# Kernel optimization log

Measured on AMD Instinct MI355X. Metric: run time of the kernel, lower is better.

## Reference

```python
import jax, jax.numpy as jnp
import numpy as np

NQ = 4          # QUANTUM_QUBITS
DIM = 2 ** NQ   # 16-dim statevector
N_LAYERS = 2
BATCH = 1 << 20


def _bit(idx, w):
    # PennyLane convention: wire 0 is the most-significant bit
    return (idx >> (NQ - 1 - w)) & 1

# Precompute CNOT permutations for the ring (w, (w+1)%NQ): flip target bit when control bit is 1.
_CNOT_PERMS = []
for w in range(NQ):
    c, t = w, (w + 1) % NQ
    perm = np.arange(DIM)
    for idx in range(DIM):
        if _bit(idx, c):
            perm[idx] = idx ^ (1 << (NQ - 1 - t))
    _CNOT_PERMS.append(jnp.asarray(perm))

# Z expectation sign vectors: sign = +1 if bit==0 else -1, per wire -> (NQ, DIM)
_Z_SIGNS = jnp.asarray(
    np.stack([[1.0 - 2.0 * _bit(idx, w) for idx in range(DIM)] for w in range(NQ)]),
    dtype=jnp.float32,
)


def _ry(t):
    c, s = jnp.cos(t / 2), jnp.sin(t / 2)
    return jnp.stack([jnp.stack([c, -s], -1), jnp.stack([s, c], -1)], -2).astype(jnp.complex64)


def _rx(t):
    c = jnp.cos(t / 2).astype(jnp.complex64)
    s = (-1j * jnp.sin(t / 2)).astype(jnp.complex64)
    return jnp.stack([jnp.stack([c, s], -1), jnp.stack([s, c], -1)], -2)


def _rz(t):
    em = jnp.exp(-0.5j * t.astype(jnp.complex64))
    ep = jnp.exp(0.5j * t.astype(jnp.complex64))
    zero = jnp.zeros_like(em)
    return jnp.stack([jnp.stack([em, zero], -1), jnp.stack([zero, ep], -1)], -2)


def _apply_batched(state, g, w):
    # state: (B, DIM); g: (B, 2, 2) per-sample gate on wire w
    s = state.reshape((-1,) + (2,) * NQ)
    s = jnp.moveaxis(s, 1 + w, 1)
    s = jnp.einsum('bij,bj...->bi...', g, s)
    s = jnp.moveaxis(s, 1, 1 + w)
    return s.reshape(-1, DIM)


def _apply_shared(state, g, w):
    # state: (B, DIM); g: (2, 2) shared gate on wire w
    s = state.reshape((-1,) + (2,) * NQ)
    s = jnp.moveaxis(s, 1 + w, 1)
    s = jnp.einsum('ij,bj...->bi...', g, s)
    s = jnp.moveaxis(s, 1, 1 + w)
    return s.reshape(-1, DIM)


def setup_inputs() -> dict:
    key = jax.random.key(0)
    kx, kw = jax.random.split(key)
    x = jax.random.normal(kx, (BATCH, NQ), dtype=jnp.float32)
    weights = jax.random.normal(kw, (N_LAYERS, NQ, 3), dtype=jnp.float32) * 0.1
    return {"x": x, "weights": weights}


def reference(x, weights):
    B = x.shape[0]
    state = jnp.zeros((B, DIM), dtype=jnp.complex64).at[:, 0].set(1.0)
    # Angle embedding: RY(x_w) on each wire (per-sample gates)
    for w in range(NQ):
        state = _apply_batched(state, _ry(x[:, w]), w)
    # Variational layers: RX, RY, RZ per wire, then CNOT ring
    for l in range(weights.shape[0]):
        for w in range(NQ):
            state = _apply_shared(state, _rx(weights[l, w, 0]), w)
            state = _apply_shared(state, _ry(weights[l, w, 1]), w)
            state = _apply_shared(state, _rz(weights[l, w, 2]), w)
        for w in range(NQ):
            state = state[:, _CNOT_PERMS[w]]
    probs = (state.real ** 2 + state.imag ** 2)  # (B, DIM)
    return probs @ _Z_SIGNS.T  # (B, NQ) <Z_w> expvals
```

## Files before the change

### kernel.cpp

```cpp
#include <hip/hip_runtime.h>

#define NQ 4
#define DIM 16

struct cplx { float r, i; };
__device__ inline cplx cmul(cplx a, cplx b) { return {a.r*b.r - a.i*b.i, a.r*b.i + a.i*b.r}; }
__device__ inline cplx cadd(cplx a, cplx b) { return {a.r + b.r, a.i + b.i}; }

__device__ inline void build9(float u, float v, float* t) {
    float su, cu, sv, cv;
    __sincosf(u, &su, &cu);
    __sincosf(v, &sv, &cv);
    t[0] = 1.f;      t[1] = cv;      t[2] = sv;
    t[3] = cu;       t[4] = cu * cv; t[5] = cu * sv;
    t[6] = su;       t[7] = su * cv; t[8] = su * sv;
}

__global__ __launch_bounds__(256) void qsim_kernel(const float4* __restrict__ x,
                                                   const float* __restrict__ wt,
                                                   float4* __restrict__ out, int half) {
    __shared__ float Ur[DIM][DIM];
    __shared__ float Ui[DIM][DIM];
    __shared__ float A[4][DIM][DIM];
    __shared__ float4 lk[81];

    int tid = blockIdx.x * blockDim.x + threadIdx.x;
    bool valid = tid < half;
    float4 xa = valid ? x[tid] : make_float4(0.f, 0.f, 0.f, 0.f);
    float4 xb = valid ? x[tid + half] : make_float4(0.f, 0.f, 0.f, 0.f);

    int col = threadIdx.x;
    if (col < DIM) {
        float ar[DIM], ai[DIM];
#pragma unroll
        for (int i = 0; i < DIM; ++i) { ar[i] = 0.f; ai[i] = 0.f; }
        ar[col] = 1.f;
        for (int l = 0; l < 2; ++l) {
            for (int q = 0; q < NQ; ++q) {
                float tx = wt[(l * 4 + q) * 3 + 0];
                float ty = wt[(l * 4 + q) * 3 + 1];
                float tz = wt[(l * 4 + q) * 3 + 2];
                float cx, sx, cy, sy, cz, sz;
                __sincosf(0.5f * tx, &sx, &cx);
                __sincosf(0.5f * ty, &sy, &cy);
                __sincosf(0.5f * tz, &sz, &cz);
                cplx Rx[2][2] = {{{cx, 0.f}, {0.f, -sx}}, {{0.f, -sx}, {cx, 0.f}}};
                cplx Ry[2][2] = {{{cy, 0.f}, {-sy, 0.f}}, {{sy, 0.f}, {cy, 0.f}}};
                cplx Rz[2][2] = {{{cz, -sz}, {0.f, 0.f}}, {{0.f, 0.f}, {cz, sz}}};
                cplx T[2][2], G[2][2];
#pragma unroll
                for (int r = 0; r < 2; ++r)
#pragma unroll
                    for (int c = 0; c < 2; ++c)
                        T[r][c] = cadd(cmul(Ry[r][0], Rx[0][c]), cmul(Ry[r][1], Rx[1][c]));
#pragma unroll
                for (int r = 0; r < 2; ++r)
#pragma unroll
                    for (int c = 0; c < 2; ++c)
                        G[r][c] = cadd(cmul(Rz[r][0], T[0][c]), cmul(Rz[r][1], T[1][c]));
                int pos = 3 - q, mask = 1 << pos;
#pragma unroll
                for (int idx = 0; idx < DIM; ++idx) {
                    if (idx & mask) continue;
                    int i1 = idx | mask;
                    cplx a0 = {ar[idx], ai[idx]}, a1 = {ar[i1], ai[i1]};
                    cplx n0 = cadd(cmul(G[0][0], a0), cmul(G[0][1], a1));
                    cplx n1 = cadd(cmul(G[1][0], a0), cmul(G[1][1], a1));
                    ar[idx] = n0.r; ai[idx] = n0.i;
                    ar[i1] = n1.r;  ai[i1] = n1.i;
                }
            }
            for (int q = 0; q < NQ; ++q) {
                int cpos = 3 - q, tpos = 3 - ((q + 1) & 3);
                int tmask = 1 << tpos;
#pragma unroll
                for (int idx = 0; idx < DIM; ++idx) {
                    if (((idx >> cpos) & 1) && !((idx >> tpos) & 1)) {
                        int i1 = idx | tmask;
                        float tr = ar[idx]; ar[idx] = ar[i1]; ar[i1] = tr;
                        float ti = ai[idx]; ai[idx] = ai[i1]; ai[i1] = ti;
                    }
                }
            }
        }
        for (int i = 0; i < DIM; ++i) { Ur[i][col] = ar[i]; Ui[i][col] = ai[i]; }
    }
    __syncthreads();

    {
        int j = threadIdx.x >> 4, k = threadIdx.x & 15;
        float a0 = 0.f, a1 = 0.f, a2 = 0.f, a3 = 0.f;
#pragma unroll
        for (int idx = 0; idx < DIM; ++idx) {
            float rr = Ur[idx][j] * Ur[idx][k] + Ui[idx][j] * Ui[idx][k];
            a0 += (idx & 8) ? -rr : rr;
            a1 += (idx & 4) ? -rr : rr;
            a2 += (idx & 2) ? -rr : rr;
            a3 += (idx & 1) ? -rr : rr;
        }
        A[0][j][k] = a0; A[1][j][k] = a1; A[2][j][k] = a2; A[3][j][k] = a3;
    }
    __syncthreads();

    for (int id = threadIdx.x; id < 4 * 81; id += blockDim.x) {
        int w = id & 3, u = id >> 2;
        int e0 = u / 27, e1 = (u / 9) % 3, e2 = (u / 3) % 3, e3 = u % 3;
        int m  = ((e0 == 2) ? 8 : 0) | ((e1 == 2) ? 4 : 0) | ((e2 == 2) ? 2 : 0) | ((e3 == 2) ? 1 : 0);
        int d1 = ((e0 == 1) ? 8 : 0) | ((e1 == 1) ? 4 : 0) | ((e2 == 1) ? 2 : 0) | ((e3 == 1) ? 1 : 0);
        float acc = 0.f;
#pragma unroll
        for (int b = 0; b < DIM; ++b) {
            float sgn = (__popc(b & d1) & 1) ? -1.f : 1.f;
            acc += sgn * A[w][b][b ^ m];
        }
        ((float*)lk)[u * 4 + w] = 0.0625f * acc;
    }
    __syncthreads();

    if (!valid) return;
    float ta[9], ua[9], tb[9], ub[9];
    build9(xa.x, xa.y, ta);  build9(xa.z, xa.w, ua);
    build9(xb.x, xb.y, tb);  build9(xb.z, xb.w, ub);

    float4 accA = make_float4(0.f, 0.f, 0.f, 0.f);
    float4 accB = make_float4(0.f, 0.f, 0.f, 0.f);
#pragma unroll
    for (int i = 0; i < 9; ++i) {
#pragma unroll
        for (int j = 0; j < 9; ++j) {
            float4 c = lk[i * 9 + j];
            float pa = ta[i] * ua[j];
            float pb = tb[i] * ub[j];
            accA.x = fmaf(c.x, pa, accA.x);
            accA.y = fmaf(c.y, pa, accA.y);
            accA.z = fmaf(c.z, pa, accA.z);
            accA.w = fmaf(c.w, pa, accA.w);
            accB.x = fmaf(c.x, pb, accB.x);
            accB.y = fmaf(c.y, pb, accB.y);
            accB.z = fmaf(c.z, pb, accB.z);
            accB.w = fmaf(c.w, pb, accB.w);
        }
    }
    out[tid] = accA;
    out[tid + half] = accB;
}

extern "C" void kernel_launch(void* const* d_in, const int* in_sizes, int n_in,
                              void* d_out, int out_size, void* d_ws, size_t ws_size,
                              hipStream_t stream) {
    const float* x = (const float*)d_in[0];
    const float* wt = (const float*)d_in[1];
    float* out = (float*)d_out;
    (void)d_ws; (void)ws_size;

    int B = in_sizes[0] / NQ;
    int half = B / 2;
    int blocks = (half + 255) / 256;
    qsim_kernel<<<blocks, 256, 0, stream>>>((const float4*)x, wt, (float4*)out, half);
}
```

Measured before the change: 83.80 us.

## Split coefficient setup into single-block kernel writing constant memory

```diff
diff --git a/kernel.cpp b/kernel.cpp
--- a/kernel.cpp
+++ b/kernel.cpp
@@ -7,7 +7,12 @@
 __device__ inline cplx cmul(cplx a, cplx b) { return {a.r*b.r - a.i*b.i, a.r*b.i + a.i*b.r}; }
 __device__ inline cplx cadd(cplx a, cplx b) { return {a.r + b.r, a.i + b.i}; }
 
-__device__ inline void build9(float u, float v, float* t) {
+template<int I> struct ic { static constexpr int v = I; };
+template<int N, typename F> __device__ __forceinline__ void sfor(F f) {
+    if constexpr (N > 0) { sfor<N - 1>(f); f(ic<N - 1>{}); }
+}
+
+__device__ __forceinline__ void build9(float u, float v, float* t) {
     float su, cu, sv, cv;
     __sincosf(u, &su, &cu);
     __sincosf(v, &sv, &cv);
@@ -16,18 +21,13 @@
     t[6] = su;       t[7] = su * cv; t[8] = su * sv;
 }
 
-__global__ __launch_bounds__(256) void qsim_kernel(const float4* __restrict__ x,
-                                                   const float* __restrict__ wt,
-                                                   float4* __restrict__ out, int half) {
+__constant__ float4 cK[81];
+
+__global__ __launch_bounds__(256) void setup_kernel(const float* __restrict__ wt,
+                                                    float* __restrict__ gk) {
     __shared__ float Ur[DIM][DIM];
     __shared__ float Ui[DIM][DIM];
     __shared__ float A[4][DIM][DIM];
-    __shared__ float4 lk[81];
-
-    int tid = blockIdx.x * blockDim.x + threadIdx.x;
-    bool valid = tid < half;
-    float4 xa = valid ? x[tid] : make_float4(0.f, 0.f, 0.f, 0.f);
-    float4 xb = valid ? x[tid + half] : make_float4(0.f, 0.f, 0.f, 0.f);
 
     int col = threadIdx.x;
     if (col < DIM) {
@@ -35,7 +35,9 @@
 #pragma unroll
         for (int i = 0; i < DIM; ++i) { ar[i] = 0.f; ai[i] = 0.f; }
         ar[col] = 1.f;
+#pragma unroll
         for (int l = 0; l < 2; ++l) {
+#pragma unroll
             for (int q = 0; q < NQ; ++q) {
                 float tx = wt[(l * 4 + q) * 3 + 0];
                 float ty = wt[(l * 4 + q) * 3 + 1];
@@ -70,6 +72,7 @@
                     ar[i1] = n1.r;  ai[i1] = n1.i;
                 }
             }
+#pragma unroll
             for (int q = 0; q < NQ; ++q) {
                 int cpos = 3 - q, tpos = 3 - ((q + 1) & 3);
                 int tmask = 1 << tpos;
@@ -83,6 +86,7 @@
                 }
             }
         }
+#pragma unroll
         for (int i = 0; i < DIM; ++i) { Ur[i][col] = ar[i]; Ui[i][col] = ai[i]; }
     }
     __syncthreads();
@@ -113,24 +117,29 @@
             float sgn = (__popc(b & d1) & 1) ? -1.f : 1.f;
             acc += sgn * A[w][b][b ^ m];
         }
-        ((float*)lk)[u * 4 + w] = 0.0625f * acc;
+        gk[u * 4 + w] = 0.0625f * acc;
     }
-    __syncthreads();
+}
 
-    if (!valid) return;
+__global__ __launch_bounds__(256) void contract_kernel(const float4* __restrict__ x,
+                                                       float4* __restrict__ out, int half) {
+    int tid = blockIdx.x * blockDim.x + threadIdx.x;
+    if (tid >= half) return;
+    float4 xa = x[tid];
+    float4 xb = x[tid + half];
+
     float ta[9], ua[9], tb[9], ub[9];
     build9(xa.x, xa.y, ta);  build9(xa.z, xa.w, ua);
     build9(xb.x, xb.y, tb);  build9(xb.z, xb.w, ub);
 
     float4 accA = make_float4(0.f, 0.f, 0.f, 0.f);
     float4 accB = make_float4(0.f, 0.f, 0.f, 0.f);
-#pragma unroll
-    for (int i = 0; i < 9; ++i) {
-#pragma unroll
-        for (int j = 0; j < 9; ++j) {
-            float4 c = lk[i * 9 + j];
-            float pa = ta[i] * ua[j];
-            float pb = tb[i] * ub[j];
+
+    sfor<9>([&](auto I) {
+        sfor<9>([&](auto J) {
+            const float4 c = cK[I.v * 9 + J.v];
+            float pa = ta[I.v] * ua[J.v];
+            float pb = tb[I.v] * ub[J.v];
             accA.x = fmaf(c.x, pa, accA.x);
             accA.y = fmaf(c.y, pa, accA.y);
             accA.z = fmaf(c.z, pa, accA.z);
@@ -139,8 +148,9 @@
             accB.y = fmaf(c.y, pb, accB.y);
             accB.z = fmaf(c.z, pb, accB.z);
             accB.w = fmaf(c.w, pb, accB.w);
-        }
-    }
+        });
+    });
+
     out[tid] = accA;
     out[tid + half] = accB;
 }
@@ -151,10 +161,15 @@
     const float* x = (const float*)d_in[0];
     const float* wt = (const float*)d_in[1];
     float* out = (float*)d_out;
-    (void)d_ws; (void)ws_size;
+    (void)d_ws; (void)ws_size; (void)n_in; (void)out_size;
+
+    static float* gk_const = nullptr;
+    if (!gk_const) hipGetSymbolAddress((void**)&gk_const, HIP_SYMBOL(cK));
 
     int B = in_sizes[0] / NQ;
     int half = B / 2;
     int blocks = (half + 255) / 256;
-    qsim_kernel<<<blocks, 256, 0, stream>>>((const float4*)x, wt, (float4*)out, half);
+
+    setup_kernel<<<1, 256, 0, stream>>>(wt, gk_const);
+    contract_kernel<<<blocks, 256, 0, stream>>>((const float4*)x, (float4*)out, half);
 }
```

After: 82.92 us. Within noise of the previous version (-1.1%).
